# Kernel optimization log

Measured on AMD Instinct MI355X. Metric: run time of the kernel, lower is better.

The kernel has to match this reference:

```python
import jax, jax.numpy as jnp
import numpy as np

SIZE_IN = 4096
SIZE_OUT = 4096
BATCH = 4096


def setup_inputs() -> dict:
    key = jax.random.key(0)
    k1, k2, k3, k4, k5, k6 = jax.random.split(key, 6)
    mu_in = jax.random.normal(k1, (BATCH, SIZE_IN), dtype=jnp.float32)
    sigma_in = jax.random.uniform(k2, (BATCH, SIZE_IN), dtype=jnp.float32)
    # parameters, initialized as in the torch module
    w_mu = 5e-05 * jax.random.normal(k3, (SIZE_IN, SIZE_OUT), dtype=jnp.float32)
    w_sigma = jax.random.uniform(k4, (SIZE_IN * SIZE_OUT,), dtype=jnp.float32,
                                 minval=-12.0, maxval=-2.2)
    b_mu = 5e-05 * jax.random.normal(k5, (SIZE_OUT,), dtype=jnp.float32)
    b_sigma = jax.random.uniform(k6, (SIZE_OUT,), dtype=jnp.float32,
                                 minval=-12.0, maxval=-10.0)
    return {"mu_in": mu_in, "sigma_in": sigma_in, "w_mu": w_mu,
            "w_sigma": w_sigma, "b_mu": b_mu, "b_sigma": b_sigma}


def reference(mu_in, sigma_in, w_mu, w_sigma, b_mu, b_sigma):
    # mean path: mu_out[b,o] = sum_i mu_in[b,i] * w_mu[i,o] + b_mu[o]
    mu_out = jnp.einsum('bi,io->bo', mu_in, w_mu) + b_mu
    # variance path: x diag(softplus(w_sigma)) x^T, per output feature.
    # Equivalent to (mu_in^2) @ softplus(w_sigma).reshape(size_in, size_out),
    # avoiding the quadratic diag_embed + bmm materialization.
    sigma_w = jax.nn.softplus(w_sigma).reshape(SIZE_IN, SIZE_OUT)
    Sigma_out = jnp.einsum('bi,io->bo', mu_in * mu_in, sigma_w) + jax.nn.softplus(b_sigma)
    # KL loss, verbatim from the torch code
    sp = jax.nn.softplus(w_sigma)
    term1 = SIZE_IN * jnp.log(sp)
    term2 = jnp.sum(jnp.abs(w_mu))
    term3 = SIZE_IN * sp
    kl_loss = -0.5 * jnp.mean(term1 - term2 - term3)
    return (mu_out, Sigma_out, kl_loss)
```

## Files before the change

### kernel.cpp

```cpp
#include <hip/hip_runtime.h>
#include <hip/hip_bf16.h>
#include <math.h>

#define M_BATCH   4096
#define K_IN      4096
#define N_OUT     4096
#define NELEM     16777216

typedef __bf16 bf16;
typedef bf16  bf16x8 __attribute__((ext_vector_type(8)));
typedef float f32x4  __attribute__((ext_vector_type(4)));
typedef float f32x16 __attribute__((ext_vector_type(16)));
typedef unsigned short u16;
typedef u16 u16x8 __attribute__((ext_vector_type(8)));

__device__ __forceinline__ float softplus_fast(float x) {
    if (x > 15.f) return x;
    const float e = __expf(x);
    if (e < 0.0883f)
        return e * (1.f + e * (-0.5f + e * 0.3333333f));
    return __logf(1.f + e);
}

__device__ __forceinline__ unsigned short f2bf_bits(float x) {
    bf16 b = (bf16)x;
    return __builtin_bit_cast(unsigned short, b);
}

__device__ __forceinline__ void gload_lds16(const void* g, void* l) {
    __builtin_amdgcn_global_load_lds(
        (__attribute__((address_space(1))) void*)g,
        (__attribute__((address_space(3))) void*)l,
        16, 0, 0);
}

__global__ __launch_bounds__(256) void prep_all(const float* __restrict__ wmu,
                                                const float* __restrict__ wsg,
                                                bf16* __restrict__ Wmu_t,
                                                bf16* __restrict__ Wsg_t,
                                                float* __restrict__ partials,
                                                const float4* __restrict__ mu,
                                                u16x8* __restrict__ A8,
                                                u16x8* __restrict__ A28) {
    __shared__ bf16 tmu[128][65];
    __shared__ bf16 tsg[128][65];
    __shared__ float wred[4][3];

    const int t   = threadIdx.x;
    const int bid = blockIdx.x;

    if (bid >= 2048) {
        const int i = (bid - 2048) * 256 + t;
        const float4 v0 = mu[2 * i];
        const float4 v1 = mu[2 * i + 1];
        u16x8 a, a2;
        a[0] = f2bf_bits(v0.x); a[1] = f2bf_bits(v0.y);
        a[2] = f2bf_bits(v0.z); a[3] = f2bf_bits(v0.w);
        a[4] = f2bf_bits(v1.x); a[5] = f2bf_bits(v1.y);
        a[6] = f2bf_bits(v1.z); a[7] = f2bf_bits(v1.w);
        a2[0] = f2bf_bits(v0.x * v0.x); a2[1] = f2bf_bits(v0.y * v0.y);
        a2[2] = f2bf_bits(v0.z * v0.z); a2[3] = f2bf_bits(v0.w * v0.w);
        a2[4] = f2bf_bits(v1.x * v1.x); a2[5] = f2bf_bits(v1.y * v1.y);
        a2[6] = f2bf_bits(v1.z * v1.z); a2[7] = f2bf_bits(v1.w * v1.w);
        A8[i]  = a;
        A28[i] = a2;
        return;
    }

    const int ti = bid >> 6;
    const int tj = bid & 63;
    const int r  = t >> 4;
    const int c4 = (t & 15) << 2;

    float s_abs = 0.f, s_sp = 0.f, s_log = 0.f;

    for (int rr = 0; rr < 128; rr += 16) {
        const int row = rr + r;
        const size_t goff = (size_t)(ti * 128 + row) * N_OUT + tj * 64 + c4;
        const float4 vm = *(const float4*)(wmu + goff);
        const float4 vs = *(const float4*)(wsg + goff);
        const float sp0 = softplus_fast(vs.x), sp1 = softplus_fast(vs.y);
        const float sp2 = softplus_fast(vs.z), sp3 = softplus_fast(vs.w);
        s_abs += fabsf(vm.x) + fabsf(vm.y) + fabsf(vm.z) + fabsf(vm.w);
        s_sp  += sp0 + sp1 + sp2 + sp3;
        s_log += __logf(sp0) + __logf(sp1) + __logf(sp2) + __logf(sp3);
        tmu[row][c4 + 0] = (bf16)vm.x; tmu[row][c4 + 1] = (bf16)vm.y;
        tmu[row][c4 + 2] = (bf16)vm.z; tmu[row][c4 + 3] = (bf16)vm.w;
        tsg[row][c4 + 0] = (bf16)sp0;  tsg[row][c4 + 1] = (bf16)sp1;
        tsg[row][c4 + 2] = (bf16)sp2;  tsg[row][c4 + 3] = (bf16)sp3;
    }
    __syncthreads();

#pragma unroll
    for (int p = 0; p < 4; ++p) {
        const int jj = p * 16 + (t >> 4);
        const int i0 = (t & 15) << 3;
        u16x8 om, os;
#pragma unroll
        for (int e = 0; e < 8; ++e) {
            om[e] = __builtin_bit_cast(unsigned short, tmu[i0 + e][jj]);
            os[e] = __builtin_bit_cast(unsigned short, tsg[i0 + e][jj]);
        }
        const size_t o = (size_t)(tj * 64 + jj) * K_IN + ti * 128 + i0;
        *(u16x8*)(Wmu_t + o) = om;
        *(u16x8*)(Wsg_t + o) = os;
    }

    float v0 = s_log, v1 = s_sp, v2 = s_abs;
#pragma unroll
    for (int off = 32; off; off >>= 1) {
        v0 += __shfl_xor(v0, off, 64);
        v1 += __shfl_xor(v1, off, 64);
        v2 += __shfl_xor(v2, off, 64);
    }
    if ((t & 63) == 0) {
        wred[t >> 6][0] = v0; wred[t >> 6][1] = v1; wred[t >> 6][2] = v2;
    }
    __syncthreads();
    if (t == 0) {
        partials[0 * 2048 + bid] = wred[0][0] + wred[1][0] + wred[2][0] + wred[3][0];
        partials[1 * 2048 + bid] = wred[0][1] + wred[1][1] + wred[2][1] + wred[3][1];
        partials[2 * 2048 + bid] = wred[0][2] + wred[1][2] + wred[2][2] + wred[3][2];
    }
}

#define MFMA32 __builtin_amdgcn_mfma_f32_32x32x16_bf16

__global__ __launch_bounds__(512, 2) void gemm_bf16(
    const bf16* __restrict__ A1,  const bf16* __restrict__ Bt1,
    const float* __restrict__ bias1, float* __restrict__ C1,
    const bf16* __restrict__ A2_, const bf16* __restrict__ Bt2,
    const float* __restrict__ bias2, float* __restrict__ C2) {

    __shared__ bf16 As[2 * 256 * 64];
    __shared__ bf16 Bs[2 * 256 * 64];

    const int z = blockIdx.z;
    const bf16*  A    = z ? A2_   : A1;
    const bf16*  Bt   = z ? Bt2   : Bt1;
    const float* bias = z ? bias2 : bias1;
    float*       C    = z ? C2    : C1;

    const int t = threadIdx.x;
    const int id   = blockIdx.y * 16 + blockIdx.x;
    const int xcd  = id & 7, cc_ = id >> 3;
    const int rowBase = (((xcd >> 1) << 2) + (cc_ >> 3)) << 8;
    const int colBase = (((xcd & 1) << 3) + (cc_ & 7)) << 8;

    const int srow   = t >> 3;
    const int schunk = (t & 7) ^ (srow & 7);
    const char* aG = (const char*)(A  + (size_t)(rowBase + srow) * K_IN + schunk * 8);
    const char* bG = (const char*)(Bt + (size_t)(colBase + srow) * K_IN + schunk * 8);
    char* aL = (char*)As + t * 16;
    char* bL = (char*)Bs + t * 16;

#define STAGE_A(kt, h, par) do {                                               \
        const size_t kb_ = (size_t)((kt) & 63) << 7;                           \
        gload_lds16(aG + kb_ + (size_t)(h) * (128 * K_IN * 2),                 \
                    aL + ((par) << 15) + ((h) << 14));                         \
        gload_lds16(aG + kb_ + (size_t)(h) * (128 * K_IN * 2) + 64 * K_IN * 2, \
                    aL + ((par) << 15) + ((h) << 14) + 8192);                  \
    } while (0)
#define STAGE_B(kt, h, par) do {                                               \
        const size_t kb_ = (size_t)((kt) & 63) << 7;                           \
        gload_lds16(bG + kb_ + (size_t)(h) * (128 * K_IN * 2),                 \
                    bL + ((par) << 15) + ((h) << 14));                         \
        gload_lds16(bG + kb_ + (size_t)(h) * (128 * K_IN * 2) + 64 * K_IN * 2, \
                    bL + ((par) << 15) + ((h) << 14) + 8192);                  \
    } while (0)

    const int lane = t & 63;
    const int wave = t >> 6;
    const int wr = wave >> 2;
    const int wc = wave & 3;
    const int fr = lane & 31;
    const int kh = lane >> 5;
    int cS[4];
#pragma unroll
    for (int s = 0; s < 4; ++s)
        cS[s] = (((s << 1) | kh) ^ (fr & 7)) << 4;
    const char* aRd = (const char*)As + ((wr << 7) + fr) * 128;
    const char* bRd = (const char*)Bs + ((wc << 6) + fr) * 128;

#define PHASE(par, q, STAGE_STMT, VM, BAR) do {                                \
        if ((q) == 0) {                                                        \
            _Pragma("unroll")                                                  \
            for (int n = 0; n < 2; ++n)                                        \
                _Pragma("unroll")                                              \
                for (int s = 0; s < 4; ++s)                                    \
                    bfrag[n][s] = *(const bf16x8*)(bRd + ((par) << 15)         \
                                                  + (n << 12) + cS[s]);        \
        }                                                                      \
        bf16x8 a_[4];                                                          \
        _Pragma("unroll")                                                      \
        for (int s = 0; s < 4; ++s)                                            \
            a_[s] = *(const bf16x8*)(aRd + ((par) << 15) + ((q) << 12) + cS[s]);\
        STAGE_STMT;                                                            \
        __builtin_amdgcn_s_setprio(1);                                         \
        _Pragma("unroll")                                                      \
        for (int s = 0; s < 4; ++s) {                                          \
            acc[q][0] = MFMA32(a_[s], bfrag[0][s], acc[q][0], 0, 0, 0);        \
            acc[q][1] = MFMA32(a_[s], bfrag[1][s], acc[q][1], 0, 0, 0);        \
        }                                                                      \
        __builtin_amdgcn_s_setprio(0);                                         \
        if (VM) {                                                              \
            asm volatile("s_waitcnt vmcnt(4)" ::: "memory");                   \
            __builtin_amdgcn_sched_barrier(0);                                 \
        }                                                                      \
        if (BAR) {                                                             \
            __builtin_amdgcn_sched_barrier(0);                                 \
            __builtin_amdgcn_s_barrier();                                      \
            __builtin_amdgcn_sched_barrier(0);                                 \
        }                                                                      \
    } while (0)

    f32x16 acc[4][2];
#pragma unroll
    for (int m = 0; m < 4; ++m)
#pragma unroll
        for (int n = 0; n < 2; ++n)
#pragma unroll
            for (int e = 0; e < 16; ++e) acc[m][n][e] = 0.f;

    STAGE_A(0, 0, 0); STAGE_A(0, 1, 0);
    STAGE_B(0, 0, 0); STAGE_B(0, 1, 0);
    STAGE_A(1, 0, 1); STAGE_A(1, 1, 1);
    STAGE_B(1, 0, 1); STAGE_B(1, 1, 1);
    asm volatile("s_waitcnt vmcnt(8)" ::: "memory");
    __builtin_amdgcn_sched_barrier(0);
    __builtin_amdgcn_s_barrier();
    __builtin_amdgcn_sched_barrier(0);

    for (int i = 0; i < 32; ++i) {
        const int kA1 = 2 * i + 1;
        const int kB0 = 2 * i + 2;
        const int kA0 = 2 * i + 2;
        const int kB1 = 2 * i + 3;
        {
            bf16x8 bfrag[2][4];
            PHASE(0, 0, STAGE_A(kA1, 0, 1), 0, 0);
            PHASE(0, 1, STAGE_A(kA1, 1, 1), 0, 1);
            PHASE(0, 2, STAGE_B(kB0, 0, 0), 0, 0);
            PHASE(0, 3, STAGE_B(kB0, 1, 0), 1, 1);
        }
        {
            bf16x8 bfrag[2][4];
            PHASE(1, 0, STAGE_A(kA0, 0, 0), 0, 0);
            PHASE(1, 1, STAGE_A(kA0, 1, 0), 0, 1);
            PHASE(1, 2, STAGE_B(kB1, 0, 1), 0, 0);
            PHASE(1, 3, STAGE_B(kB1, 1, 1), 1, 1);
        }
    }

    asm volatile("s_waitcnt vmcnt(0)" ::: "memory");

#pragma unroll
    for (int n = 0; n < 2; ++n) {
        const int c = colBase + (wc << 6) + (n << 5) + fr;
        float b = bias[c];
        if (z) b = softplus_fast(b);
#pragma unroll
        for (int m = 0; m < 4; ++m) {
            const int rb = rowBase + (wr << 7) + (m << 5) + (kh << 2);
#pragma unroll
            for (int reg = 0; reg < 16; ++reg) {
                const int row = rb + (reg & 3) + ((reg >> 2) << 3);
                C[(size_t)row * N_OUT + c] = acc[m][n][reg] + b;
            }
        }
    }
#undef STAGE_A
#undef STAGE_B
#undef PHASE
}

__global__ __launch_bounds__(256) void kl_finish(const float* __restrict__ partials,
                                                 const int n,
                                                 float* __restrict__ out) {
    __shared__ double red[256];
    const int t = threadIdx.x;
    double sums[3];
    for (int v = 0; v < 3; v++) {
        double a = 0.0;
        for (int i = t; i < n; i += 256) a += (double)partials[v * n + i];
        red[t] = a;
        __syncthreads();
        for (int s = 128; s > 0; s >>= 1) {
            if (t < s) red[t] += red[t + s];
            __syncthreads();
        }
        sums[v] = red[0];
        __syncthreads();
    }
    if (t == 0) {
        const double mean_log = sums[0] / 16777216.0;
        const double mean_sp  = sums[1] / 16777216.0;
        const double kl = -0.5 * (4096.0 * mean_log - sums[2] - 4096.0 * mean_sp);
        out[0] = (float)kl;
    }
}

__global__ void fb_partials(const float* __restrict__ wmu,
                            const float* __restrict__ wsg,
                            float* __restrict__ partials) {
    __shared__ float red[256];
    const int t = threadIdx.x;
    float s_abs = 0.f, s_sp = 0.f, s_log = 0.f;
    for (int i = blockIdx.x * 256 + t; i < NELEM; i += 1024 * 256) {
        s_abs += fabsf(wmu[i]);
        const float sp = softplus_fast(wsg[i]);
        s_sp += sp;
        s_log += __logf(sp);
    }
    float vals[3] = { s_log, s_sp, s_abs };
    for (int v = 0; v < 3; v++) {
        __syncthreads();
        red[t] = vals[v];
        __syncthreads();
        for (int s = 128; s > 0; s >>= 1) {
            if (t < s) red[t] += red[t + s];
            __syncthreads();
        }
        if (t == 0) partials[v * 1024 + blockIdx.x] = red[0];
    }
}

__global__ void fb_gemm(const float* __restrict__ A,
                        const float* __restrict__ Wm,
                        const float* __restrict__ Ws,
                        const float* __restrict__ bmu,
                        const float* __restrict__ bsg,
                        float* __restrict__ Cmu,
                        float* __restrict__ Csg) {
    __shared__ float As_[16][17], Bm[16][17], Bs_[16][17];
    const int tx = threadIdx.x, ty = threadIdx.y;
    const int row = blockIdx.y * 16 + ty;
    const int col = blockIdx.x * 16 + tx;
    float am = 0.f, as = 0.f;
    for (int k0 = 0; k0 < K_IN; k0 += 16) {
        As_[ty][tx] = A[(size_t)row * K_IN + k0 + tx];
        Bm[ty][tx]  = Wm[(size_t)(k0 + ty) * N_OUT + col];
        Bs_[ty][tx] = softplus_fast(Ws[(size_t)(k0 + ty) * N_OUT + col]);
        __syncthreads();
#pragma unroll
        for (int kk = 0; kk < 16; kk++) {
            const float av = As_[ty][kk];
            am += av * Bm[kk][tx];
            as += av * av * Bs_[kk][tx];
        }
        __syncthreads();
    }
    Cmu[(size_t)row * N_OUT + col] = am + bmu[col];
    Csg[(size_t)row * N_OUT + col] = as + softplus_fast(bsg[col]);
}

extern "C" void kernel_launch(void* const* d_in, const int* in_sizes, int n_in,
                              void* d_out, int out_size, void* d_ws, size_t ws_size,
                              hipStream_t stream) {
    const float* mu_in   = (const float*)d_in[0];
    const float* w_mu    = (const float*)d_in[2];
    const float* w_sigma = (const float*)d_in[3];
    const float* b_mu    = (const float*)d_in[4];
    const float* b_sigma = (const float*)d_in[5];

    float* out_mu  = (float*)d_out;
    float* out_sig = out_mu + (size_t)NELEM;
    float* out_kl  = out_mu + 2 * (size_t)NELEM;

    const size_t mat  = (size_t)NELEM;
    const size_t need = mat * 2 * 4  + 3 * 4096 * sizeof(float);

    if (ws_size >= need) {
        bf16* A      = (bf16*)d_ws;
        bf16* A2     = A + mat;
        bf16* Wmu_t  = A2 + mat;
        bf16* Wsg_t  = Wmu_t + mat;
        float* parts = (float*)(Wsg_t + mat);

        prep_all<<<2048 + 8192, 256, 0, stream>>>(
            w_mu, w_sigma, Wmu_t, Wsg_t, parts,
            (const float4*)mu_in, (u16x8*)A, (u16x8*)A2);
        gemm_bf16<<<dim3(16, 16, 2), 512, 0, stream>>>(
            A, Wmu_t, b_mu, out_mu, A2, Wsg_t, b_sigma, out_sig);
        kl_finish<<<1, 256, 0, stream>>>(parts, 2048, out_kl);
    } else {
        float* parts = (float*)d_ws;
        fb_partials<<<1024, 256, 0, stream>>>(w_mu, w_sigma, parts);
        fb_gemm<<<dim3(256, 256), dim3(16, 16), 0, stream>>>(
            mu_in, w_mu, w_sigma, b_mu, b_sigma, out_mu, out_sig);
        kl_finish<<<1, 256, 0, stream>>>(parts, 1024, out_kl);
    }
}
```

Measured before the change: 556.7 us.

## Double GEMM workgroup to 1024 threads with 64x64 per-wave tiles

The bf16 GEMM block is grown from 8 to 16 waves while keeping the 256x256 block tile. Each wave now computes a 64x64 sub-tile with a 2x2 accumulator array instead of 128x64. Each thread issues one global-to-LDS load per stage instead of two, and the vmcnt waits are halved to match. The aim is more waves to hide latency and lower per-wave register pressure. The trade-off is a worse MFMA-to-LDS-read ratio per wave. The launch bounds of (1024, 4) also request occupancy the compiler may try to satisfy by capping registers.

```diff
diff --git a/kernel.cpp b/kernel.cpp
--- a/kernel.cpp
+++ b/kernel.cpp
@@ -126,7 +126,7 @@
 
 #define MFMA32 __builtin_amdgcn_mfma_f32_32x32x16_bf16
 
-__global__ __launch_bounds__(512, 2) void gemm_bf16(
+__global__ __launch_bounds__(1024, 4) void gemm_bf16(
     const bf16* __restrict__ A1,  const bf16* __restrict__ Bt1,
     const float* __restrict__ bias1, float* __restrict__ C1,
     const bf16* __restrict__ A2_, const bf16* __restrict__ Bt2,
@@ -154,20 +154,12 @@
     char* aL = (char*)As + t * 16;
     char* bL = (char*)Bs + t * 16;
 
-#define STAGE_A(kt, h, par) do {                                               \
-        const size_t kb_ = (size_t)((kt) & 63) << 7;                           \
-        gload_lds16(aG + kb_ + (size_t)(h) * (128 * K_IN * 2),                 \
-                    aL + ((par) << 15) + ((h) << 14));                         \
-        gload_lds16(aG + kb_ + (size_t)(h) * (128 * K_IN * 2) + 64 * K_IN * 2, \
-                    aL + ((par) << 15) + ((h) << 14) + 8192);                  \
-    } while (0)
-#define STAGE_B(kt, h, par) do {                                               \
-        const size_t kb_ = (size_t)((kt) & 63) << 7;                           \
-        gload_lds16(bG + kb_ + (size_t)(h) * (128 * K_IN * 2),                 \
-                    bL + ((par) << 15) + ((h) << 14));                         \
-        gload_lds16(bG + kb_ + (size_t)(h) * (128 * K_IN * 2) + 64 * K_IN * 2, \
-                    bL + ((par) << 15) + ((h) << 14) + 8192);                  \
-    } while (0)
+#define STAGE_A(kt, h, par)                                                    \
+    gload_lds16(aG + ((size_t)((kt) & 63) << 7) + (size_t)(h) * (128 * K_IN * 2), \
+                aL + ((par) << 15) + ((h) << 14))
+#define STAGE_B(kt, h, par)                                                    \
+    gload_lds16(bG + ((size_t)((kt) & 63) << 7) + (size_t)(h) * (128 * K_IN * 2), \
+                bL + ((par) << 15) + ((h) << 14))
 
     const int lane = t & 63;
     const int wave = t >> 6;
@@ -179,32 +171,38 @@
 #pragma unroll
     for (int s = 0; s < 4; ++s)
         cS[s] = (((s << 1) | kh) ^ (fr & 7)) << 4;
-    const char* aRd = (const char*)As + ((wr << 7) + fr) * 128;
+    const char* aRd = (const char*)As + ((wr << 6) + fr) * 128;
     const char* bRd = (const char*)Bs + ((wc << 6) + fr) * 128;
+
+#define DS_A(par, m, ks) (*(const bf16x8*)(aRd + ((par) << 15) + ((m) << 12) + cS[ks]))
+#define DS_B(par, n, ks) (*(const bf16x8*)(bRd + ((par) << 15) + ((n) << 12) + cS[ks]))
 
 #define PHASE(par, q, STAGE_STMT, VM, BAR) do {                                \
         if ((q) == 0) {                                                        \
             _Pragma("unroll")                                                  \
-            for (int n = 0; n < 2; ++n)                                        \
+            for (int pp = 0; pp < 2; ++pp)                                     \
                 _Pragma("unroll")                                              \
-                for (int s = 0; s < 4; ++s)                                    \
-                    bfrag[n][s] = *(const bf16x8*)(bRd + ((par) << 15)         \
-                                                  + (n << 12) + cS[s]);        \
+                for (int n = 0; n < 2; ++n)                                    \
+                    _Pragma("unroll")                                          \
+                    for (int j = 0; j < 2; ++j)                                \
+                        bfrag[pp][n][j] = DS_B(par, n, pp * 2 + j);            \
         }                                                                      \
-        bf16x8 a_[4];                                                          \
+        bf16x8 a_[2];                                                          \
         _Pragma("unroll")                                                      \
-        for (int s = 0; s < 4; ++s)                                            \
-            a_[s] = *(const bf16x8*)(aRd + ((par) << 15) + ((q) << 12) + cS[s]);\
+        for (int j = 0; j < 2; ++j)                                            \
+            a_[j] = DS_A(par, (q) & 1, ((q) >> 1) * 2 + j);                    \
         STAGE_STMT;                                                            \
         __builtin_amdgcn_s_setprio(1);                                         \
         _Pragma("unroll")                                                      \
-        for (int s = 0; s < 4; ++s) {                                          \
-            acc[q][0] = MFMA32(a_[s], bfrag[0][s], acc[q][0], 0, 0, 0);        \
-            acc[q][1] = MFMA32(a_[s], bfrag[1][s], acc[q][1], 0, 0, 0);        \
+        for (int j = 0; j < 2; ++j) {                                          \
+            acc[(q) & 1][0] = MFMA32(a_[j], bfrag[(q) >> 1][0][j],             \
+                                     acc[(q) & 1][0], 0, 0, 0);                \
+            acc[(q) & 1][1] = MFMA32(a_[j], bfrag[(q) >> 1][1][j],             \
+                                     acc[(q) & 1][1], 0, 0, 0);                \
         }                                                                      \
         __builtin_amdgcn_s_setprio(0);                                         \
         if (VM) {                                                              \
-            asm volatile("s_waitcnt vmcnt(4)" ::: "memory");                   \
+            asm volatile("s_waitcnt vmcnt(2)" ::: "memory");                   \
             __builtin_amdgcn_sched_barrier(0);                                 \
         }                                                                      \
         if (BAR) {                                                             \
@@ -214,19 +212,21 @@
         }                                                                      \
     } while (0)
 
-    f32x16 acc[4][2];
-#pragma unroll
-    for (int m = 0; m < 4; ++m)
+    f32x16 acc[2][2];
+#pragma unroll
+    for (int m = 0; m < 2; ++m)
 #pragma unroll
         for (int n = 0; n < 2; ++n)
 #pragma unroll
             for (int e = 0; e < 16; ++e) acc[m][n][e] = 0.f;
+
+    bf16x8 bfrag[2][2][2];
 
     STAGE_A(0, 0, 0); STAGE_A(0, 1, 0);
     STAGE_B(0, 0, 0); STAGE_B(0, 1, 0);
     STAGE_A(1, 0, 1); STAGE_A(1, 1, 1);
     STAGE_B(1, 0, 1); STAGE_B(1, 1, 1);
-    asm volatile("s_waitcnt vmcnt(8)" ::: "memory");
+    asm volatile("s_waitcnt vmcnt(4)" ::: "memory");
     __builtin_amdgcn_sched_barrier(0);
     __builtin_amdgcn_s_barrier();
     __builtin_amdgcn_sched_barrier(0);
@@ -236,20 +236,14 @@
         const int kB0 = 2 * i + 2;
         const int kA0 = 2 * i + 2;
         const int kB1 = 2 * i + 3;
-        {
-            bf16x8 bfrag[2][4];
-            PHASE(0, 0, STAGE_A(kA1, 0, 1), 0, 0);
-            PHASE(0, 1, STAGE_A(kA1, 1, 1), 0, 1);
-            PHASE(0, 2, STAGE_B(kB0, 0, 0), 0, 0);
-            PHASE(0, 3, STAGE_B(kB0, 1, 0), 1, 1);
-        }
-        {
-            bf16x8 bfrag[2][4];
-            PHASE(1, 0, STAGE_A(kA0, 0, 0), 0, 0);
-            PHASE(1, 1, STAGE_A(kA0, 1, 0), 0, 1);
-            PHASE(1, 2, STAGE_B(kB1, 0, 1), 0, 0);
-            PHASE(1, 3, STAGE_B(kB1, 1, 1), 1, 1);
-        }
+        PHASE(0, 0, STAGE_A(kA1, 0, 1), 0, 0);
+        PHASE(0, 1, STAGE_A(kA1, 1, 1), 0, 1);
+        PHASE(0, 2, STAGE_B(kB0, 0, 0), 0, 0);
+        PHASE(0, 3, STAGE_B(kB0, 1, 0), 1, 1);
+        PHASE(1, 0, STAGE_A(kA0, 0, 0), 0, 0);
+        PHASE(1, 1, STAGE_A(kA0, 1, 0), 0, 1);
+        PHASE(1, 2, STAGE_B(kB1, 0, 1), 0, 0);
+        PHASE(1, 3, STAGE_B(kB1, 1, 1), 1, 1);
     }
 
     asm volatile("s_waitcnt vmcnt(0)" ::: "memory");
@@ -260,8 +254,8 @@
         float b = bias[c];
         if (z) b = softplus_fast(b);
 #pragma unroll
-        for (int m = 0; m < 4; ++m) {
-            const int rb = rowBase + (wr << 7) + (m << 5) + (kh << 2);
+        for (int m = 0; m < 2; ++m) {
+            const int rb = rowBase + (wr << 6) + (m << 5) + (kh << 2);
 #pragma unroll
             for (int reg = 0; reg < 16; ++reg) {
                 const int row = rb + (reg & 3) + ((reg >> 2) << 3);
@@ -271,6 +265,8 @@
     }
 #undef STAGE_A
 #undef STAGE_B
+#undef DS_A
+#undef DS_B
 #undef PHASE
 }
 
@@ -380,7 +376,7 @@
         prep_all<<<2048 + 8192, 256, 0, stream>>>(
             w_mu, w_sigma, Wmu_t, Wsg_t, parts,
             (const float4*)mu_in, (u16x8*)A, (u16x8*)A2);
-        gemm_bf16<<<dim3(16, 16, 2), 512, 0, stream>>>(
+        gemm_bf16<<<dim3(16, 16, 2), 1024, 0, stream>>>(
             A, Wmu_t, b_mu, out_mu, A2, Wsg_t, b_sigma, out_sig);
         kl_finish<<<1, 256, 0, stream>>>(parts, 2048, out_kl);
     } else {
```

After: 719.0 us. +29.1%, slower.

## Load GEMM B operand directly from global into double-buffered registers, bypassing LDS

Applied to the files above, without the earlier changes.

The B tile is no longer staged through shared memory. Each wave loads its own B fragments straight from global memory into two register buffers, prefetching the next k-tile while the current one feeds the MFMAs. One mid-iteration barrier per half is dropped and the vmcnt wait thresholds are retuned. This removes LDS traffic and LDS capacity for B, but it duplicates global and L2 reads across waves that share columns, uses poorly coalesced 16-byte per-lane row accesses, and adds about 64 VGPRs of register pressure under a 512x2 launch bound, which risks spills or lower occupancy.

```diff
diff --git a/kernel.cpp b/kernel.cpp
--- a/kernel.cpp
+++ b/kernel.cpp
@@ -133,7 +133,6 @@
     const float* __restrict__ bias2, float* __restrict__ C2) {
 
     __shared__ bf16 As[2 * 256 * 64];
-    __shared__ bf16 Bs[2 * 256 * 64];
 
     const int z = blockIdx.z;
     const bf16*  A    = z ? A2_   : A1;
@@ -149,10 +148,8 @@
 
     const int srow   = t >> 3;
     const int schunk = (t & 7) ^ (srow & 7);
-    const char* aG = (const char*)(A  + (size_t)(rowBase + srow) * K_IN + schunk * 8);
-    const char* bG = (const char*)(Bt + (size_t)(colBase + srow) * K_IN + schunk * 8);
+    const char* aG = (const char*)(A + (size_t)(rowBase + srow) * K_IN + schunk * 8);
     char* aL = (char*)As + t * 16;
-    char* bL = (char*)Bs + t * 16;
 
 #define STAGE_A(kt, h, par) do {                                               \
         const size_t kb_ = (size_t)((kt) & 63) << 7;                           \
@@ -161,13 +158,6 @@
         gload_lds16(aG + kb_ + (size_t)(h) * (128 * K_IN * 2) + 64 * K_IN * 2, \
                     aL + ((par) << 15) + ((h) << 14) + 8192);                  \
     } while (0)
-#define STAGE_B(kt, h, par) do {                                               \
-        const size_t kb_ = (size_t)((kt) & 63) << 7;                           \
-        gload_lds16(bG + kb_ + (size_t)(h) * (128 * K_IN * 2),                 \
-                    bL + ((par) << 15) + ((h) << 14));                         \
-        gload_lds16(bG + kb_ + (size_t)(h) * (128 * K_IN * 2) + 64 * K_IN * 2, \
-                    bL + ((par) << 15) + ((h) << 14) + 8192);                  \
-    } while (0)
 
     const int lane = t & 63;
     const int wave = t >> 6;
@@ -180,17 +170,21 @@
     for (int s = 0; s < 4; ++s)
         cS[s] = (((s << 1) | kh) ^ (fr & 7)) << 4;
     const char* aRd = (const char*)As + ((wr << 7) + fr) * 128;
-    const char* bRd = (const char*)Bs + ((wc << 6) + fr) * 128;
-
-#define PHASE(par, q, STAGE_STMT, VM, BAR) do {                                \
-        if ((q) == 0) {                                                        \
+
+    const bf16* bGr = Bt + (size_t)(colBase + (wc << 6) + fr) * K_IN + (kh << 3);
+
+#define LOAD_B(buf, ktN) do {                                                  \
+        __builtin_amdgcn_sched_barrier(0);                                     \
+        const size_t kb_ = (size_t)((ktN) & 63) << 6;                          \
+        _Pragma("unroll")                                                      \
+        for (int n = 0; n < 2; ++n)                                            \
             _Pragma("unroll")                                                  \
-            for (int n = 0; n < 2; ++n)                                        \
-                _Pragma("unroll")                                              \
-                for (int s = 0; s < 4; ++s)                                    \
-                    bfrag[n][s] = *(const bf16x8*)(bRd + ((par) << 15)         \
-                                                  + (n << 12) + cS[s]);        \
-        }                                                                      \
+            for (int s = 0; s < 4; ++s)                                        \
+                buf[n][s] = *(const bf16x8*)(bGr + (size_t)n * (32 * K_IN)     \
+                                             + kb_ + (s << 4));                \
+    } while (0)
+
+#define PHASE(par, q, bufB, STAGE_STMT, POST_STMT, VM, BAR) do {               \
         bf16x8 a_[4];                                                          \
         _Pragma("unroll")                                                      \
         for (int s = 0; s < 4; ++s)                                            \
@@ -199,12 +193,13 @@
         __builtin_amdgcn_s_setprio(1);                                         \
         _Pragma("unroll")                                                      \
         for (int s = 0; s < 4; ++s) {                                          \
-            acc[q][0] = MFMA32(a_[s], bfrag[0][s], acc[q][0], 0, 0, 0);        \
-            acc[q][1] = MFMA32(a_[s], bfrag[1][s], acc[q][1], 0, 0, 0);        \
+            acc[q][0] = MFMA32(a_[s], bufB[0][s], acc[q][0], 0, 0, 0);         \
+            acc[q][1] = MFMA32(a_[s], bufB[1][s], acc[q][1], 0, 0, 0);         \
         }                                                                      \
         __builtin_amdgcn_s_setprio(0);                                         \
+        POST_STMT;                                                             \
         if (VM) {                                                              \
-            asm volatile("s_waitcnt vmcnt(4)" ::: "memory");                   \
+            asm volatile("s_waitcnt vmcnt(8)" ::: "memory");                   \
             __builtin_amdgcn_sched_barrier(0);                                 \
         }                                                                      \
         if (BAR) {                                                             \
@@ -213,6 +208,7 @@
             __builtin_amdgcn_sched_barrier(0);                                 \
         }                                                                      \
     } while (0)
+#define NOPST (void)0
 
     f32x16 acc[4][2];
 #pragma unroll
@@ -222,10 +218,12 @@
 #pragma unroll
             for (int e = 0; e < 16; ++e) acc[m][n][e] = 0.f;
 
+    bf16x8 b0[2][4], b1[2][4];
+
     STAGE_A(0, 0, 0); STAGE_A(0, 1, 0);
-    STAGE_B(0, 0, 0); STAGE_B(0, 1, 0);
     STAGE_A(1, 0, 1); STAGE_A(1, 1, 1);
-    STAGE_B(1, 0, 1); STAGE_B(1, 1, 1);
+    LOAD_B(b0, 0);
+    LOAD_B(b1, 1);
     asm volatile("s_waitcnt vmcnt(8)" ::: "memory");
     __builtin_amdgcn_sched_barrier(0);
     __builtin_amdgcn_s_barrier();
@@ -233,26 +231,21 @@
 
     for (int i = 0; i < 32; ++i) {
         const int kA1 = 2 * i + 1;
+        const int kA0 = 2 * i + 2;
         const int kB0 = 2 * i + 2;
-        const int kA0 = 2 * i + 2;
         const int kB1 = 2 * i + 3;
-        {
-            bf16x8 bfrag[2][4];
-            PHASE(0, 0, STAGE_A(kA1, 0, 1), 0, 0);
-            PHASE(0, 1, STAGE_A(kA1, 1, 1), 0, 1);
-            PHASE(0, 2, STAGE_B(kB0, 0, 0), 0, 0);
-            PHASE(0, 3, STAGE_B(kB0, 1, 0), 1, 1);
-        }
-        {
-            bf16x8 bfrag[2][4];
-            PHASE(1, 0, STAGE_A(kA0, 0, 0), 0, 0);
-            PHASE(1, 1, STAGE_A(kA0, 1, 0), 0, 1);
-            PHASE(1, 2, STAGE_B(kB1, 0, 1), 0, 0);
-            PHASE(1, 3, STAGE_B(kB1, 1, 1), 1, 1);
-        }
+        PHASE(0, 0, b0, STAGE_A(kA1, 0, 1), NOPST, 0, 0);
+        PHASE(0, 1, b0, STAGE_A(kA1, 1, 1), NOPST, 0, 0);
+        PHASE(0, 2, b0, NOPST, NOPST, 0, 0);
+        PHASE(0, 3, b0, NOPST, LOAD_B(b0, kB0), 1, 1);
+        PHASE(1, 0, b1, STAGE_A(kA0, 0, 0), NOPST, 0, 0);
+        PHASE(1, 1, b1, STAGE_A(kA0, 1, 0), NOPST, 0, 0);
+        PHASE(1, 2, b1, NOPST, NOPST, 0, 0);
+        PHASE(1, 3, b1, NOPST, LOAD_B(b1, kB1), 1, 1);
     }
 
     asm volatile("s_waitcnt vmcnt(0)" ::: "memory");
+    asm volatile("" :: "v"(b0[0][0]), "v"(b0[1][3]), "v"(b1[0][0]), "v"(b1[1][3]));
 
 #pragma unroll
     for (int n = 0; n < 2; ++n) {
@@ -270,8 +263,9 @@
         }
     }
 #undef STAGE_A
-#undef STAGE_B
+#undef LOAD_B
 #undef PHASE
+#undef NOPST
 }
 
 __global__ __launch_bounds__(256) void kl_finish(const float* __restrict__ partials,
```

New measurement: 645.9 us. 16.0% more time.
